# Kernel tuning notes

Measured on AMD Instinct MI355X. Metric: run time of the kernel, lower is better.

The kernel has to match this reference:

```python
import jax, jax.numpy as jnp
import numpy as np
import math

N_NODES = 50000
N_EDGES = 800000
D = 128
ALPHA = 0.1
BETA = 0.5


def setup_inputs() -> dict:
    key = jax.random.key(0)
    k = jax.random.split(key, 7)
    h = jax.random.normal(k[0], (N_NODES, D), dtype=jnp.float32)
    h0 = jax.random.normal(k[1], (N_NODES, D), dtype=jnp.float32)
    edge_row = jnp.sort(jax.random.randint(k[2], (N_EDGES,), 0, N_NODES, dtype=jnp.int32))
    edge_col = jax.random.randint(k[3], (N_EDGES,), 0, N_NODES, dtype=jnp.int32)
    edge_vals = jax.random.uniform(k[4], (N_EDGES,), dtype=jnp.float32)
    # nn.Linear(input_dim, output_dim): W is [out, in], b is [out]
    bound = 1.0 / math.sqrt(D)
    W = jax.random.uniform(k[5], (D, D), minval=-bound, maxval=bound, dtype=jnp.float32)
    b = jax.random.uniform(k[6], (D,), minval=-bound, maxval=bound, dtype=jnp.float32)
    return {"h": h, "h0": h0, "edge_row": edge_row, "edge_col": edge_col,
            "edge_vals": edge_vals, "W": W, "b": b, "l": 4}


def reference(h, h0, edge_row, edge_col, edge_vals, W, b, l):
    theta = math.log(BETA / l + 1.0)
    # sparse adj @ h : gather source features, scale by edge value, scatter-add to rows
    msgs = edge_vals[:, None] * h[edge_col]          # [E, D]
    hi = jax.ops.segment_sum(msgs, edge_row, num_segments=N_NODES)  # [N, D]
    support = (1.0 - ALPHA) * hi + ALPHA * h0
    lin = support @ W.T + b
    return theta * lin + (1.0 - theta) * support
```

## Files before the change

### kernel.cpp

```cpp
#include <hip/hip_runtime.h>
#include <hip/hip_bf16.h>
#include <math.h>

#define NN 50000
#define DD 128
#define ALPHA 0.1f
#define BETA 0.5f

typedef __attribute__((ext_vector_type(8))) short short8;
typedef __attribute__((ext_vector_type(4))) float floatx4;
typedef _Float16 h2 __attribute__((ext_vector_type(2)));

__device__ __forceinline__ float bf16lo(unsigned u) {
    return __uint_as_float(u << 16);
}
__device__ __forceinline__ float bf16hi(unsigned u) {
    return __uint_as_float(u & 0xffff0000u);
}
__device__ __forceinline__ unsigned pkh(float a, float b) {
    h2 p = {(_Float16)a, (_Float16)b};
    return __builtin_bit_cast(unsigned, p);
}
__device__ __forceinline__ h2 as_h2(unsigned u) {
    return __builtin_bit_cast(h2, u);
}

__global__ __launch_bounds__(256) void prep_kernel(
    const int* __restrict__ edge_row, int E, int* __restrict__ rp,
    const float* __restrict__ h, ushort* __restrict__ hh,
    const float* __restrict__ W, ushort* __restrict__ wf)
{
    const int t = blockIdx.x * 256 + threadIdx.x;

    if (hh != nullptr && t < NN * DD / 8) {
        const float4 v0 = *reinterpret_cast<const float4*>(h + (size_t)t * 8);
        const float4 v1 = *reinterpret_cast<const float4*>(h + (size_t)t * 8 + 4);
        uint4 o;
        o.x = pkh(v0.x, v0.y);
        o.y = pkh(v0.z, v0.w);
        o.z = pkh(v1.x, v1.y);
        o.w = pkh(v1.z, v1.w);
        *reinterpret_cast<uint4*>(hh + (size_t)t * 8) = o;
    }

    if (wf != nullptr && t < DD * DD / 4) {
        const float4 v = *reinterpret_cast<const float4*>(W + (size_t)t * 4);
        uint2 of;
        of.x = pkh(v.x, v.y);
        of.y = pkh(v.z, v.w);
        *reinterpret_cast<uint2*>(wf + (size_t)t * 4) = of;
    }

    if (t <= E) {
        if (t == 0) {
            int r0 = edge_row[0];
            for (int r = 0; r <= r0; ++r) rp[r] = 0;
        } else if (t == E) {
            int rl = edge_row[E - 1];
            for (int r = rl + 1; r <= NN; ++r) rp[r] = E;
        } else {
            int rprev = edge_row[t - 1];
            int rcur  = edge_row[t];
            for (int r = rprev + 1; r <= rcur; ++r) rp[r] = t;
        }
    }
}

__global__ __launch_bounds__(256, 6) void fused16(
    const ushort* __restrict__ hh, const float* __restrict__ h0,
    const int* __restrict__ edge_col, const float* __restrict__ edge_vals,
    const int* __restrict__ rp, const ushort* __restrict__ wf,
    const float* __restrict__ b, const int* __restrict__ lptr,
    float* __restrict__ out)
{
    __shared__ float  sS[16][132];
    __shared__ ushort sA[16][136];

    const int tid  = threadIdx.x;
    const int wave = tid >> 6;
    const int lane = tid & 63;
    const int g    = lane >> 4;
    const int li   = lane & 15;
    const int r0   = blockIdx.x * 16;

    const int lv = *lptr;
    const float theta  = logf(BETA / (float)lv + 1.0f);
    const float mtheta = 1.0f - theta;

    #pragma unroll 1
    for (int q = 0; q < 4; ++q) {
        const int ri = wave * 4 + q;
        const int r  = r0 + ri;
        const int e0 = rp[r], e1 = rp[r + 1];

        h2 a0 = {0, 0}, a1 = {0, 0}, a2 = {0, 0}, a3 = {0, 0};

        for (int eb = e0; eb < e1; eb += 16) {
            #pragma unroll
            for (int u = 0; u < 4; ++u) {
                const int e  = eb + u * 4 + g;
                const int ee = min(e, e1 - 1);
                const int   c = edge_col[ee];
                const float v = (e < e1) ? edge_vals[ee] : 0.0f;
                const uint4 hv = *reinterpret_cast<const uint4*>(
                    hh + (size_t)c * DD + li * 8);
                const _Float16 vh = (_Float16)v;
                const h2 vv = {vh, vh};
                a0 += as_h2(hv.x) * vv;
                a1 += as_h2(hv.y) * vv;
                a2 += as_h2(hv.z) * vv;
                a3 += as_h2(hv.w) * vv;
            }
        }

        float acc[8];
        acc[0] = (float)a0.x; acc[1] = (float)a0.y;
        acc[2] = (float)a1.x; acc[3] = (float)a1.y;
        acc[4] = (float)a2.x; acc[5] = (float)a2.y;
        acc[6] = (float)a3.x; acc[7] = (float)a3.y;

        #pragma unroll
        for (int j = 0; j < 8; ++j) {
            acc[j] += __shfl_xor(acc[j], 16);
            acc[j] += __shfl_xor(acc[j], 32);
        }

        if (g == 0) {
            const float4 h0a = *reinterpret_cast<const float4*>(
                h0 + (size_t)r * DD + li * 8);
            const float4 h0b = *reinterpret_cast<const float4*>(
                h0 + (size_t)r * DD + li * 8 + 4);
            float sup[8];
            sup[0] = fmaf(1.0f - ALPHA, acc[0], ALPHA * h0a.x);
            sup[1] = fmaf(1.0f - ALPHA, acc[1], ALPHA * h0a.y);
            sup[2] = fmaf(1.0f - ALPHA, acc[2], ALPHA * h0a.z);
            sup[3] = fmaf(1.0f - ALPHA, acc[3], ALPHA * h0a.w);
            sup[4] = fmaf(1.0f - ALPHA, acc[4], ALPHA * h0b.x);
            sup[5] = fmaf(1.0f - ALPHA, acc[5], ALPHA * h0b.y);
            sup[6] = fmaf(1.0f - ALPHA, acc[6], ALPHA * h0b.z);
            sup[7] = fmaf(1.0f - ALPHA, acc[7], ALPHA * h0b.w);
            *reinterpret_cast<float4*>(&sS[ri][li * 8]) =
                make_float4(sup[0], sup[1], sup[2], sup[3]);
            *reinterpret_cast<float4*>(&sS[ri][li * 8 + 4]) =
                make_float4(sup[4], sup[5], sup[6], sup[7]);
            uint4 pk;
            pk.x = pkh(sup[0], sup[1]);
            pk.y = pkh(sup[2], sup[3]);
            pk.z = pkh(sup[4], sup[5]);
            pk.w = pkh(sup[6], sup[7]);
            *reinterpret_cast<uint4*>(&sA[ri][li * 8]) = pk;
        }
    }
    __syncthreads();

    const int la = lane & 15;
    const int k0 = (lane >> 4) * 8;

    floatx4 facc[2];
    facc[0] = (floatx4){0.f, 0.f, 0.f, 0.f};
    facc[1] = (floatx4){0.f, 0.f, 0.f, 0.f};

    #pragma unroll
    for (int s = 0; s < 4; ++s) {
        const int k = s * 32 + k0;
        const short8 af = *reinterpret_cast<const short8*>(&sA[la][k]);
        #pragma unroll
        for (int t = 0; t < 2; ++t) {
            const int col = wave * 32 + t * 16 + la;
            const short8 bf = *reinterpret_cast<const short8*>(
                wf + (size_t)col * DD + k);
            facc[t] = __builtin_amdgcn_mfma_f32_16x16x32_f16(af, bf, facc[t], 0, 0, 0);
        }
    }

    const int rg = (lane >> 4) * 4;
    #pragma unroll
    for (int t = 0; t < 2; ++t) {
        const int c  = wave * 32 + t * 16 + la;
        const float bb = b[c];
        #pragma unroll
        for (int j = 0; j < 4; ++j) {
            const int rl = rg + j;
            out[(size_t)(r0 + rl) * DD + c] =
                theta * (facc[t][j] + bb) + mtheta * sS[rl][c];
        }
    }
}

__global__ __launch_bounds__(256, 6) void agg_fp32(
    const float* __restrict__ h, const float* __restrict__ h0,
    const int* __restrict__ edge_col, const float* __restrict__ edge_vals,
    const int* __restrict__ rp, float* __restrict__ io)
{
    const int wave = threadIdx.x >> 6;
    const int lane = threadIdx.x & 63;
    const int p    = lane >> 5;
    const int li   = lane & 31;
    const int r    = blockIdx.x * 4 + wave;
    if (r >= NN) return;

    const int e0 = rp[r], e1 = rp[r + 1];

    float4 A[4];
    #pragma unroll
    for (int u = 0; u < 4; ++u) A[u] = make_float4(0.f, 0.f, 0.f, 0.f);

    for (int eb = e0; eb < e1; eb += 8) {
        #pragma unroll
        for (int u = 0; u < 4; ++u) {
            const int e  = eb + 2 * u + p;
            const int ee = min(e, e1 - 1);
            const int   c = edge_col[ee];
            const float v = (e < e1) ? edge_vals[ee] : 0.0f;
            const float4 hv =
                *reinterpret_cast<const float4*>(h + (size_t)c * DD + li * 4);
            A[u].x = fmaf(v, hv.x, A[u].x);
            A[u].y = fmaf(v, hv.y, A[u].y);
            A[u].z = fmaf(v, hv.z, A[u].z);
            A[u].w = fmaf(v, hv.w, A[u].w);
        }
    }
    float4 s;
    s.x = (A[0].x + A[1].x) + (A[2].x + A[3].x);
    s.y = (A[0].y + A[1].y) + (A[2].y + A[3].y);
    s.z = (A[0].z + A[1].z) + (A[2].z + A[3].z);
    s.w = (A[0].w + A[1].w) + (A[2].w + A[3].w);
    s.x += __shfl_xor(s.x, 32);
    s.y += __shfl_xor(s.y, 32);
    s.z += __shfl_xor(s.z, 32);
    s.w += __shfl_xor(s.w, 32);

    if (p == 0) {
        const float4 h0v =
            *reinterpret_cast<const float4*>(h0 + (size_t)r * DD + li * 4);
        float4 sup;
        sup.x = fmaf(1.0f - ALPHA, s.x, ALPHA * h0v.x);
        sup.y = fmaf(1.0f - ALPHA, s.y, ALPHA * h0v.y);
        sup.z = fmaf(1.0f - ALPHA, s.z, ALPHA * h0v.z);
        sup.w = fmaf(1.0f - ALPHA, s.w, ALPHA * h0v.w);
        *reinterpret_cast<float4*>(io + (size_t)r * DD + li * 4) = sup;
    }
}

#define RPB 64
#define SPAD 132
#define WPAD 136

__global__ __launch_bounds__(512, 4) void lin_kernel(
    float* io, const float* __restrict__ W, const float* __restrict__ b,
    const int* __restrict__ lptr)
{
    __shared__ float sS[RPB][SPAD];
    __shared__ __hip_bfloat16 sWt[DD][WPAD];

    const int tid = threadIdx.x;
    const int r0  = blockIdx.x * RPB;
    const int tr  = tid >> 4;
    const int tc  = tid & 15;

    const int lv = *lptr;
    const float theta  = logf(BETA / (float)lv + 1.0f);
    const float mtheta = 1.0f - theta;

    for (int i = tid * 4; i < DD * DD; i += 512 * 4) {
        const float4 w4 = *reinterpret_cast<const float4*>(W + i);
        const int o = i >> 7;
        const int k = i & 127;
        sWt[k + 0][o] = __float2bfloat16(w4.x);
        sWt[k + 1][o] = __float2bfloat16(w4.y);
        sWt[k + 2][o] = __float2bfloat16(w4.z);
        sWt[k + 3][o] = __float2bfloat16(w4.w);
    }

    for (int idx = tid; idx < RPB * 32; idx += 512) {
        const int row = idx >> 5;
        const int q   = idx & 31;
        const int rr  = r0 + row;
        const float4 v = (rr < NN)
            ? *reinterpret_cast<const float4*>(io + (size_t)rr * DD + q * 4)
            : make_float4(0.f, 0.f, 0.f, 0.f);
        *reinterpret_cast<float4*>(&sS[row][q * 4]) = v;
    }
    __syncthreads();

    float acc[2][8];
    #pragma unroll
    for (int i = 0; i < 2; ++i)
        #pragma unroll
        for (int j = 0; j < 8; ++j) acc[i][j] = 0.f;

    for (int k = 0; k < DD; k += 4) {
        const float4 a0 = *reinterpret_cast<const float4*>(&sS[tr * 2 + 0][k]);
        const float4 a1 = *reinterpret_cast<const float4*>(&sS[tr * 2 + 1][k]);
        const float aa0[4] = {a0.x, a0.y, a0.z, a0.w};
        const float aa1[4] = {a1.x, a1.y, a1.z, a1.w};
        #pragma unroll
        for (int kk = 0; kk < 4; ++kk) {
            const uint4 wr = *reinterpret_cast<const uint4*>(&sWt[k + kk][tc * 8]);
            float w[8];
            w[0] = bf16lo(wr.x); w[1] = bf16hi(wr.x);
            w[2] = bf16lo(wr.y); w[3] = bf16hi(wr.y);
            w[4] = bf16lo(wr.z); w[5] = bf16hi(wr.z);
            w[6] = bf16lo(wr.w); w[7] = bf16hi(wr.w);
            #pragma unroll
            for (int j = 0; j < 8; ++j) {
                acc[0][j] = fmaf(aa0[kk], w[j], acc[0][j]);
                acc[1][j] = fmaf(aa1[kk], w[j], acc[1][j]);
            }
        }
    }

    #pragma unroll
    for (int i = 0; i < 2; ++i) {
        const int ri = tr * 2 + i;
        const int rr = r0 + ri;
        if (rr >= NN) continue;
        #pragma unroll
        for (int j4 = 0; j4 < 2; ++j4) {
            const int cc = tc * 8 + j4 * 4;
            const float4 bv  = *reinterpret_cast<const float4*>(&b[cc]);
            const float4 sup = *reinterpret_cast<const float4*>(&sS[ri][cc]);
            float4 o4;
            o4.x = theta * (acc[i][j4 * 4 + 0] + bv.x) + mtheta * sup.x;
            o4.y = theta * (acc[i][j4 * 4 + 1] + bv.y) + mtheta * sup.y;
            o4.z = theta * (acc[i][j4 * 4 + 2] + bv.z) + mtheta * sup.z;
            o4.w = theta * (acc[i][j4 * 4 + 3] + bv.w) + mtheta * sup.w;
            *reinterpret_cast<float4*>(io + (size_t)rr * DD + cc) = o4;
        }
    }
}

extern "C" void kernel_launch(void* const* d_in, const int* in_sizes, int n_in,
                              void* d_out, int out_size, void* d_ws, size_t ws_size,
                              hipStream_t stream) {
    const float* h         = (const float*)d_in[0];
    const float* h0        = (const float*)d_in[1];
    const int*   edge_row  = (const int*)d_in[2];
    const int*   edge_col  = (const int*)d_in[3];
    const float* edge_vals = (const float*)d_in[4];
    const float* W         = (const float*)d_in[5];
    const float* b         = (const float*)d_in[6];
    const int*   lptr      = (const int*)d_in[7];
    const int E = in_sizes[2];

    char* wsb = (char*)d_ws;
    const size_t sz_hh = (size_t)NN * DD * sizeof(ushort);
    const size_t sz_w  = (size_t)DD * DD * sizeof(ushort);
    int*    rp = (int*)wsb;
    ushort* hh = (ushort*)(wsb + (1 << 18));
    ushort* wf = (ushort*)(wsb + (1 << 18) + sz_hh);
    float*  io = (float*)d_out;

    const size_t need = (size_t)(1 << 18) + sz_hh + sz_w;

    const int nT = (NN * DD / 8 > E + 1) ? NN * DD / 8 : E + 1;
    const int gridP = (nT + 255) / 256;

    if (ws_size >= need) {
        prep_kernel<<<gridP, 256, 0, stream>>>(edge_row, E, rp, h, hh, W, wf);
        fused16<<<NN / 16, 256, 0, stream>>>(
            hh, h0, edge_col, edge_vals, rp, wf, b, lptr, io);
    } else {
        prep_kernel<<<gridP, 256, 0, stream>>>(edge_row, E, rp, h,
                                               nullptr, W, nullptr);
        agg_fp32<<<(NN + 3) / 4, 256, 0, stream>>>(h, h0, edge_col, edge_vals, rp, io);
        lin_kernel<<<(NN + RPB - 1) / RPB, 512, 0, stream>>>(io, W, b, lptr);
    }
}
```

Before: 64.00 us.

## Use one wave per row with 1024-thread blocks in fused aggregation kernel

The fused kernel now launches 16 waves per block so each wave aggregates a single row, instead of 4 waves each looping over 4 rows serially. The fp32 support staging buffer is dropped and the epilogue reads support back from the fp16 shared tile. Only 8 of the 16 waves take part in the MFMA linear stage, each computing one 16-column tile. This raises memory-level parallelism for the gather, at the cost of half the waves idling during the GEMM stage and lower precision in the residual term.

New measurement: 66.46 us. 3.8% more time.

```diff
diff --git a/kernel.cpp b/kernel.cpp
--- a/kernel.cpp
+++ b/kernel.cpp
@@ -66,14 +66,13 @@
     }
 }
 
-__global__ __launch_bounds__(256, 6) void fused16(
+__global__ __launch_bounds__(1024, 8) void fused16w(
     const ushort* __restrict__ hh, const float* __restrict__ h0,
     const int* __restrict__ edge_col, const float* __restrict__ edge_vals,
     const int* __restrict__ rp, const ushort* __restrict__ wf,
     const float* __restrict__ b, const int* __restrict__ lptr,
     float* __restrict__ out)
 {
-    __shared__ float  sS[16][132];
     __shared__ ushort sA[16][136];
 
     const int tid  = threadIdx.x;
@@ -82,108 +81,94 @@
     const int g    = lane >> 4;
     const int li   = lane & 15;
     const int r0   = blockIdx.x * 16;
+    const int r    = r0 + wave;
 
     const int lv = *lptr;
     const float theta  = logf(BETA / (float)lv + 1.0f);
     const float mtheta = 1.0f - theta;
 
-    #pragma unroll 1
-    for (int q = 0; q < 4; ++q) {
-        const int ri = wave * 4 + q;
-        const int r  = r0 + ri;
-        const int e0 = rp[r], e1 = rp[r + 1];
-
-        h2 a0 = {0, 0}, a1 = {0, 0}, a2 = {0, 0}, a3 = {0, 0};
-
-        for (int eb = e0; eb < e1; eb += 16) {
-            #pragma unroll
-            for (int u = 0; u < 4; ++u) {
-                const int e  = eb + u * 4 + g;
-                const int ee = min(e, e1 - 1);
-                const int   c = edge_col[ee];
-                const float v = (e < e1) ? edge_vals[ee] : 0.0f;
-                const uint4 hv = *reinterpret_cast<const uint4*>(
-                    hh + (size_t)c * DD + li * 8);
-                const _Float16 vh = (_Float16)v;
-                const h2 vv = {vh, vh};
-                a0 += as_h2(hv.x) * vv;
-                a1 += as_h2(hv.y) * vv;
-                a2 += as_h2(hv.z) * vv;
-                a3 += as_h2(hv.w) * vv;
-            }
-        }
-
-        float acc[8];
-        acc[0] = (float)a0.x; acc[1] = (float)a0.y;
-        acc[2] = (float)a1.x; acc[3] = (float)a1.y;
-        acc[4] = (float)a2.x; acc[5] = (float)a2.y;
-        acc[6] = (float)a3.x; acc[7] = (float)a3.y;
-
-        #pragma unroll
-        for (int j = 0; j < 8; ++j) {
-            acc[j] += __shfl_xor(acc[j], 16);
-            acc[j] += __shfl_xor(acc[j], 32);
-        }
-
-        if (g == 0) {
-            const float4 h0a = *reinterpret_cast<const float4*>(
-                h0 + (size_t)r * DD + li * 8);
-            const float4 h0b = *reinterpret_cast<const float4*>(
-                h0 + (size_t)r * DD + li * 8 + 4);
-            float sup[8];
-            sup[0] = fmaf(1.0f - ALPHA, acc[0], ALPHA * h0a.x);
-            sup[1] = fmaf(1.0f - ALPHA, acc[1], ALPHA * h0a.y);
-            sup[2] = fmaf(1.0f - ALPHA, acc[2], ALPHA * h0a.z);
-            sup[3] = fmaf(1.0f - ALPHA, acc[3], ALPHA * h0a.w);
-            sup[4] = fmaf(1.0f - ALPHA, acc[4], ALPHA * h0b.x);
-            sup[5] = fmaf(1.0f - ALPHA, acc[5], ALPHA * h0b.y);
-            sup[6] = fmaf(1.0f - ALPHA, acc[6], ALPHA * h0b.z);
-            sup[7] = fmaf(1.0f - ALPHA, acc[7], ALPHA * h0b.w);
-            *reinterpret_cast<float4*>(&sS[ri][li * 8]) =
-                make_float4(sup[0], sup[1], sup[2], sup[3]);
-            *reinterpret_cast<float4*>(&sS[ri][li * 8 + 4]) =
-                make_float4(sup[4], sup[5], sup[6], sup[7]);
-            uint4 pk;
-            pk.x = pkh(sup[0], sup[1]);
-            pk.y = pkh(sup[2], sup[3]);
-            pk.z = pkh(sup[4], sup[5]);
-            pk.w = pkh(sup[6], sup[7]);
-            *reinterpret_cast<uint4*>(&sA[ri][li * 8]) = pk;
-        }
+    const int e0 = rp[r], e1 = rp[r + 1];
+
+    h2 a0 = {0, 0}, a1 = {0, 0}, a2 = {0, 0}, a3 = {0, 0};
+
+    for (int eb = e0; eb < e1; eb += 16) {
+        #pragma unroll
+        for (int u = 0; u < 4; ++u) {
+            const int e  = eb + u * 4 + g;
+            const int ee = min(e, e1 - 1);
+            const int   c = edge_col[ee];
+            const float v = (e < e1) ? edge_vals[ee] : 0.0f;
+            const uint4 hv = *reinterpret_cast<const uint4*>(
+                hh + (size_t)c * DD + li * 8);
+            const _Float16 vh = (_Float16)v;
+            const h2 vv = {vh, vh};
+            a0 += as_h2(hv.x) * vv;
+            a1 += as_h2(hv.y) * vv;
+            a2 += as_h2(hv.z) * vv;
+            a3 += as_h2(hv.w) * vv;
+        }
+    }
+
+    float acc[8];
+    acc[0] = (float)a0.x; acc[1] = (float)a0.y;
+    acc[2] = (float)a1.x; acc[3] = (float)a1.y;
+    acc[4] = (float)a2.x; acc[5] = (float)a2.y;
+    acc[6] = (float)a3.x; acc[7] = (float)a3.y;
+
+    #pragma unroll
+    for (int j = 0; j < 8; ++j) {
+        acc[j] += __shfl_xor(acc[j], 16);
+        acc[j] += __shfl_xor(acc[j], 32);
+    }
+
+    if (g == 0) {
+        const float4 h0a = *reinterpret_cast<const float4*>(
+            h0 + (size_t)r * DD + li * 8);
+        const float4 h0b = *reinterpret_cast<const float4*>(
+            h0 + (size_t)r * DD + li * 8 + 4);
+        float sup[8];
+        sup[0] = fmaf(1.0f - ALPHA, acc[0], ALPHA * h0a.x);
+        sup[1] = fmaf(1.0f - ALPHA, acc[1], ALPHA * h0a.y);
+        sup[2] = fmaf(1.0f - ALPHA, acc[2], ALPHA * h0a.z);
+        sup[3] = fmaf(1.0f - ALPHA, acc[3], ALPHA * h0a.w);
+        sup[4] = fmaf(1.0f - ALPHA, acc[4], ALPHA * h0b.x);
+        sup[5] = fmaf(1.0f - ALPHA, acc[5], ALPHA * h0b.y);
+        sup[6] = fmaf(1.0f - ALPHA, acc[6], ALPHA * h0b.z);
+        sup[7] = fmaf(1.0f - ALPHA, acc[7], ALPHA * h0b.w);
+        uint4 pk;
+        pk.x = pkh(sup[0], sup[1]);
+        pk.y = pkh(sup[2], sup[3]);
+        pk.z = pkh(sup[4], sup[5]);
+        pk.w = pkh(sup[6], sup[7]);
+        *reinterpret_cast<uint4*>(&sA[wave][li * 8]) = pk;
     }
     __syncthreads();
+
+    if (wave >= 8) return;
 
     const int la = lane & 15;
     const int k0 = (lane >> 4) * 8;
-
-    floatx4 facc[2];
-    facc[0] = (floatx4){0.f, 0.f, 0.f, 0.f};
-    facc[1] = (floatx4){0.f, 0.f, 0.f, 0.f};
+    const int c  = wave * 16 + la;
+
+    floatx4 facc = (floatx4){0.f, 0.f, 0.f, 0.f};
 
     #pragma unroll
     for (int s = 0; s < 4; ++s) {
         const int k = s * 32 + k0;
         const short8 af = *reinterpret_cast<const short8*>(&sA[la][k]);
-        #pragma unroll
-        for (int t = 0; t < 2; ++t) {
-            const int col = wave * 32 + t * 16 + la;
-            const short8 bf = *reinterpret_cast<const short8*>(
-                wf + (size_t)col * DD + k);
-            facc[t] = __builtin_amdgcn_mfma_f32_16x16x32_f16(af, bf, facc[t], 0, 0, 0);
-        }
+        const short8 bf = *reinterpret_cast<const short8*>(
+            wf + (size_t)c * DD + k);
+        facc = __builtin_amdgcn_mfma_f32_16x16x32_f16(af, bf, facc, 0, 0, 0);
     }
 
     const int rg = (lane >> 4) * 4;
-    #pragma unroll
-    for (int t = 0; t < 2; ++t) {
-        const int c  = wave * 32 + t * 16 + la;
-        const float bb = b[c];
-        #pragma unroll
-        for (int j = 0; j < 4; ++j) {
-            const int rl = rg + j;
-            out[(size_t)(r0 + rl) * DD + c] =
-                theta * (facc[t][j] + bb) + mtheta * sS[rl][c];
-        }
+    const float bb = b[c];
+    #pragma unroll
+    for (int j = 0; j < 4; ++j) {
+        const int rl = rg + j;
+        const float sup = (float)(*reinterpret_cast<const _Float16*>(&sA[rl][c]));
+        out[(size_t)(r0 + rl) * DD + c] =
+            theta * (facc[j] + bb) + mtheta * sup;
     }
 }
 
@@ -358,7 +343,7 @@
 
     if (ws_size >= need) {
         prep_kernel<<<gridP, 256, 0, stream>>>(edge_row, E, rp, h, hh, W, wf);
-        fused16<<<NN / 16, 256, 0, stream>>>(
+        fused16w<<<NN / 16, 1024, 0, stream>>>(
             hh, h0, edge_col, edge_vals, rp, wf, b, lptr, io);
     } else {
         prep_kernel<<<gridP, 256, 0, stream>>>(edge_row, E, rp, h,
```
